# Kernel tuning notes

Hardware: AMD Instinct MI355X
Metric: run time of the kernel (lower is better)

The kernel has to match this reference:

```python
import jax, jax.numpy as jnp
import numpy as np

N = 100000   # n_nodes
E = 1600000  # n_edges (avg degree 16)
IN, HID, OUT = 128, 128, 64


def setup_inputs() -> dict:
    key = jax.random.key(0)
    k0, k1, k2, k3 = jax.random.split(key, 4)
    x = jax.random.normal(k0, (N, IN), dtype=jnp.float32)
    edge_index = jax.random.randint(k1, (2, E), 0, N, dtype=jnp.int32)
    # Glorot-ish init for GCNConv weights, zero bias (PyG default bias=True)
    W1 = jax.random.normal(k2, (IN, HID), dtype=jnp.float32) * (1.0 / np.sqrt(IN))
    b1 = jnp.zeros((HID,), dtype=jnp.float32)
    W2 = jax.random.normal(k3, (HID, OUT), dtype=jnp.float32) * (1.0 / np.sqrt(HID))
    b2 = jnp.zeros((OUT,), dtype=jnp.float32)
    return {"x": x, "W1": W1, "b1": b1, "W2": W2, "b2": b2, "edge_index": edge_index}


def gcn_layer(x, W, b, src, dst):
    """PyG GCNConv: add self-loops, symmetric deg^{-1/2} normalization,
    linear transform, scatter-add aggregation at dst, plus bias."""
    n = x.shape[0]
    h = x @ W                                   # [n, d_out]
    loops = jnp.arange(n, dtype=src.dtype)
    s = jnp.concatenate([src, loops])           # sources incl. self-loops
    d = jnp.concatenate([dst, loops])           # targets incl. self-loops
    deg = jax.ops.segment_sum(jnp.ones_like(d, dtype=h.dtype), d, num_segments=n)
    dinv = jnp.where(deg > 0, jax.lax.rsqrt(deg), 0.0)
    norm = dinv[s] * dinv[d]                    # [E+n]
    msg = h[s] * norm[:, None]                  # gather + scale
    out = jax.ops.segment_sum(msg, d, num_segments=n)  # scatter-add
    return out + b


def reference(x, W1, b1, W2, b2, edge_index):
    src, dst = edge_index[0], edge_index[1]
    h = jax.nn.relu(gcn_layer(x, W1, b1, src, dst))
    return gcn_layer(h, W2, b2, src, dst)
```

## Files before the change

### kernel.cpp

```cpp
#include <hip/hip_runtime.h>

#define NNODES 100000
#define NEDGES 1600000
#define IND 128
#define HIDD 128
#define OUTD 64

#define BSHIFT 8
#define BSIZE  256
#define NBUCK  ((NNODES + BSIZE - 1) / BSIZE)
#define SLACK  4800
#define SEG_CAP 5120
#define BIN_EPB 4096
#define BINB   ((NEDGES + BIN_EPB - 1) / BIN_EPB)
#define WTB    ((IND * HIDD + HIDD * OUTD + 255) / 256)
#define GEMMB  ((NNODES + 127) / 128)

typedef unsigned int  uint32;
typedef __attribute__((ext_vector_type(8))) short short8;
typedef __attribute__((ext_vector_type(4))) float floatx4;
typedef __attribute__((ext_vector_type(4))) unsigned int uivec4;
typedef __attribute__((ext_vector_type(4))) float fvec4;

__device__ __forceinline__ unsigned short f2bf(float f) {
    union { float f; uint32 u; } x; x.f = f;
    uint32 u = x.u;
    return (unsigned short)((u + 0x7fffu + ((u >> 16) & 1u)) >> 16);
}
__device__ __forceinline__ float bflo(uint32 u) {
    union { uint32 i; float f; } x; x.i = u << 16; return x.f;
}
__device__ __forceinline__ float bfhi(uint32 u) {
    union { uint32 i; float f; } x; x.i = u & 0xffff0000u; return x.f;
}

__global__ void k_bin(const int* __restrict__ src, const int* __restrict__ dst,
                      int* __restrict__ bcnt, uint32* __restrict__ staging, int e,
                      const float* __restrict__ W1, const float* __restrict__ W2,
                      unsigned short* __restrict__ wt1, unsigned short* __restrict__ wt2) {
    const int tid = threadIdx.x;
    if (blockIdx.x >= BINB) {
        int idx = (blockIdx.x - BINB) * 256 + tid;
        if (idx < IND * HIDD) {
            int k = idx / HIDD, m = idx - k * HIDD;
            wt1[m * IND + k] = f2bf(W1[idx]);
        } else {
            int j = idx - IND * HIDD;
            if (j < HIDD * OUTD) {
                int k = j / OUTD, m = j - k * OUTD;
                wt2[m * HIDD + k] = f2bf(W2[j]);
            }
        }
        return;
    }

    __shared__ int lh[NBUCK];
    __shared__ int lcur[NBUCK];
    for (int i = tid; i < NBUCK; i += 256) lh[i] = 0;
    __syncthreads();

    const int start = blockIdx.x * BIN_EPB;
    const int4* d4 = (const int4*)dst;
    const int4* s4 = (const int4*)src;

    int4 dv[4], sv[4];
    bool val[4];
#pragma unroll
    for (int k = 0; k < 4; k++) {
        int off = start + 4 * (k * 256 + tid);
        val[k] = off < e;
        if (val[k]) { dv[k] = d4[off >> 2]; sv[k] = s4[off >> 2]; }
    }

#pragma unroll
    for (int k = 0; k < 4; k++) {
        if (val[k]) {
            atomicAdd(&lh[dv[k].x >> BSHIFT], 1);
            atomicAdd(&lh[dv[k].y >> BSHIFT], 1);
            atomicAdd(&lh[dv[k].z >> BSHIFT], 1);
            atomicAdd(&lh[dv[k].w >> BSHIFT], 1);
        }
    }
    __syncthreads();

    for (int i = tid; i < NBUCK; i += 256)
        lcur[i] = lh[i] ? atomicAdd(&bcnt[i], lh[i]) : 0;
    __syncthreads();

#pragma unroll
    for (int k = 0; k < 4; k++) {
        if (val[k]) {
            int d, s, b, pos;
            d = dv[k].x; s = sv[k].x; b = d >> BSHIFT;
            pos = atomicAdd(&lcur[b], 1);
            if (pos < SLACK) staging[b * SLACK + pos] = ((uint32)(d & (BSIZE - 1)) << 17) | (uint32)s;
            d = dv[k].y; s = sv[k].y; b = d >> BSHIFT;
            pos = atomicAdd(&lcur[b], 1);
            if (pos < SLACK) staging[b * SLACK + pos] = ((uint32)(d & (BSIZE - 1)) << 17) | (uint32)s;
            d = dv[k].z; s = sv[k].z; b = d >> BSHIFT;
            pos = atomicAdd(&lcur[b], 1);
            if (pos < SLACK) staging[b * SLACK + pos] = ((uint32)(d & (BSIZE - 1)) << 17) | (uint32)s;
            d = dv[k].w; s = sv[k].w; b = d >> BSHIFT;
            pos = atomicAdd(&lcur[b], 1);
            if (pos < SLACK) staging[b * SLACK + pos] = ((uint32)(d & (BSIZE - 1)) << 17) | (uint32)s;
        }
    }
}

__global__ __launch_bounds__(256)
void k_fill3(const uint32* __restrict__ staging, const int* __restrict__ bcnt,
             int* __restrict__ row_ptr, int* __restrict__ csr_src,
             float* __restrict__ dinv, int n) {
    __shared__ int nc[BSIZE];
    __shared__ int lcur[BSIZE];
    __shared__ int red[256];
    __shared__ int wsum[4];
    __shared__ int seg[SEG_CAP];
    const int b = blockIdx.x;
    const int base = b << BSHIFT;
    const int tid = threadIdx.x;

    nc[tid] = 0;

    int t0 = (tid < b) ? bcnt[tid] : 0;
    int t1 = (tid + 256 < b) ? bcnt[tid + 256] : 0;
    red[tid] = t0 + t1;
    __syncthreads();
    for (int off = 128; off > 0; off >>= 1) {
        if (tid < off) red[tid] += red[tid + off];
        __syncthreads();
    }
    const int r0 = red[0];

    const uint32* st = staging + (size_t)b * SLACK;
    const int cnt = bcnt[b];
    for (int i = tid; i < cnt; i += 256)
        atomicAdd(&nc[st[i] >> 17], 1);
    __syncthreads();

    const int lane = tid & 63;
    const int w = tid >> 6;
    int dg = nc[tid];
    int v = dg;
#pragma unroll
    for (int off = 1; off < 64; off <<= 1) {
        int t = __shfl_up(v, off);
        if (lane >= off) v += t;
    }
    if (lane == 63) wsum[w] = v;
    __syncthreads();
    if (tid == 0) {
        int a = 0;
#pragma unroll
        for (int i = 0; i < 4; i++) { int t = wsum[i]; wsum[i] = a; a += t; }
    }
    __syncthreads();
    const int inc = v + wsum[w];
    const int ex = inc - dg;
    const int vnode = base + tid;
    if (vnode < n) {
        row_ptr[vnode] = r0 + ex;
        dinv[vnode] = rsqrtf((float)(dg + 1));
    }
    lcur[tid] = ex;
    if (b == NBUCK - 1 && tid == 255) row_ptr[n] = r0 + inc;
    __syncthreads();

    for (int i = tid; i < cnt; i += 256) {
        uint32 p = st[i];
        int dl = (int)(p >> 17);
        int s  = (int)(p & 0x1FFFFu);
        int pos = atomicAdd(&lcur[dl], 1);
        if (pos < SEG_CAP) seg[pos] = s;
        else               csr_src[r0 + pos] = s;
    }
    __syncthreads();
    int lim = min(cnt, SEG_CAP);
    for (int i = tid; i < lim; i += 256) csr_src[r0 + i] = seg[i];
}

template<int K, int M, bool ABF16>
__launch_bounds__(512)
__global__ void gemm_mfma(const void* __restrict__ Ap, const unsigned short* __restrict__ WT,
                          const float* __restrict__ dinv, unsigned short* __restrict__ C, int n) {
    constexpr int KP = K + 8;
    constexpr int NT = M / 16;
    __shared__ unsigned short Asl[128 * KP];
    __shared__ unsigned short Wsl[M * KP];

    const int tid = threadIdx.x;
    const int row0 = blockIdx.x * 128;

    {
        constexpr int SEG = (K * 2) / 16;
        const uint4* srcp = (const uint4*)WT;
        for (int idx = tid; idx < M * SEG; idx += 512) {
            int r = idx / SEG, s = idx - r * SEG;
            *(uint4*)(Wsl + r * KP + s * 8) = srcp[idx];
        }
    }
    if constexpr (ABF16) {
        constexpr int U4R = K / 8;
        const unsigned short* Ab = (const unsigned short*)Ap;
        for (int idx = tid; idx < 128 * U4R; idx += 512) {
            int r = idx / U4R, s = idx - r * U4R;
            int grow = row0 + r; if (grow >= n) grow = n - 1;
            *(uint4*)(Asl + r * KP + s * 8) = *(const uint4*)(Ab + (size_t)grow * K + s * 8);
        }
    } else {
        constexpr int F4R = K / 4;
        const float* Af = (const float*)Ap;
        for (int idx = tid; idx < 128 * F4R; idx += 512) {
            int r = idx / F4R, s = idx - r * F4R;
            int grow = row0 + r; if (grow >= n) grow = n - 1;
            float4 v = *(const float4*)(Af + (size_t)grow * K + s * 4);
            uint32 p0 = (uint32)f2bf(v.x) | ((uint32)f2bf(v.y) << 16);
            uint32 p1 = (uint32)f2bf(v.z) | ((uint32)f2bf(v.w) << 16);
            *(uint2*)(Asl + r * KP + s * 4) = make_uint2(p0, p1);
        }
    }
    __syncthreads();

    const int lane = tid & 63;
    const int wave = tid >> 6;
    const int mm = lane & 15;
    const int qq = lane >> 4;

    floatx4 acc[NT];
#pragma unroll
    for (int t = 0; t < NT; t++) acc[t] = (floatx4){0.f, 0.f, 0.f, 0.f};

#pragma unroll
    for (int kc = 0; kc < K / 32; kc++) {
        short8 a = *(const short8*)(Asl + (wave * 16 + mm) * KP + kc * 32 + qq * 8);
#pragma unroll
        for (int t = 0; t < NT; t++) {
            short8 b = *(const short8*)(Wsl + (t * 16 + mm) * KP + kc * 32 + qq * 8);
            acc[t] = __builtin_amdgcn_mfma_f32_16x16x32_bf16(a, b, acc[t], 0, 0, 0);
        }
    }

#pragma unroll
    for (int r = 0; r < 4; r++) {
        int grow = row0 + wave * 16 + qq * 4 + r;
        if (grow < n) {
            float dv = dinv[grow];
#pragma unroll
            for (int t = 0; t < NT; t++)
                C[(size_t)grow * M + t * 16 + mm] = f2bf(acc[t][r] * dv);
        }
    }
}

__launch_bounds__(256)
__global__ void gather_gemm(const unsigned short* __restrict__ h,
                            const int* __restrict__ row_ptr,
                            const int* __restrict__ csr_src,
                            const float* __restrict__ dinv,
                            const float* __restrict__ bias1,
                            const unsigned short* __restrict__ WT2,
                            unsigned short* __restrict__ C2, int n) {
    constexpr int K  = HIDD;
    constexpr int KP = K + 8;
    constexpr int M2 = OUTD;
    __shared__ unsigned short Atl[16 * KP];
    __shared__ unsigned short Wsl[M2 * KP];

    const int tid = threadIdx.x;

    {
        constexpr int SEG = (K * 2) / 16;
        const uint4* srcp = (const uint4*)WT2;
        for (int idx = tid; idx < M2 * SEG; idx += 256) {
            int r = idx / SEG, s = idx - r * SEG;
            *(uint4*)(Wsl + r * KP + s * 8) = srcp[idx];
        }
    }

    const int g = tid >> 4;
    const int l = tid & 15;
    const int v0 = blockIdx.x * 16;
    const int v = v0 + g;

    uint4 pk = make_uint4(0u, 0u, 0u, 0u);
    if (v < n) {
        const float dv = dinv[v];
        float acc[8];
        {
            uint4 u = *(const uint4*)(h + (size_t)v * K + l * 8);
            acc[0] = bflo(u.x); acc[1] = bfhi(u.x);
            acc[2] = bflo(u.y); acc[3] = bfhi(u.y);
            acc[4] = bflo(u.z); acc[5] = bfhi(u.z);
            acc[6] = bflo(u.w); acc[7] = bfhi(u.w);
        }

        int j   = row_ptr[v];
        int end = row_ptr[v + 1];
        for (; j + 3 < end; j += 4) {
            int s0 = csr_src[j];
            int s1 = csr_src[j + 1];
            int s2 = csr_src[j + 2];
            int s3 = csr_src[j + 3];
            uint4 u0 = *(const uint4*)(h + (size_t)s0 * K + l * 8);
            uint4 u1 = *(const uint4*)(h + (size_t)s1 * K + l * 8);
            uint4 u2 = *(const uint4*)(h + (size_t)s2 * K + l * 8);
            uint4 u3 = *(const uint4*)(h + (size_t)s3 * K + l * 8);
            acc[0] += (bflo(u0.x) + bflo(u1.x)) + (bflo(u2.x) + bflo(u3.x));
            acc[1] += (bfhi(u0.x) + bfhi(u1.x)) + (bfhi(u2.x) + bfhi(u3.x));
            acc[2] += (bflo(u0.y) + bflo(u1.y)) + (bflo(u2.y) + bflo(u3.y));
            acc[3] += (bfhi(u0.y) + bfhi(u1.y)) + (bfhi(u2.y) + bfhi(u3.y));
            acc[4] += (bflo(u0.z) + bflo(u1.z)) + (bflo(u2.z) + bflo(u3.z));
            acc[5] += (bfhi(u0.z) + bfhi(u1.z)) + (bfhi(u2.z) + bfhi(u3.z));
            acc[6] += (bflo(u0.w) + bflo(u1.w)) + (bflo(u2.w) + bflo(u3.w));
            acc[7] += (bfhi(u0.w) + bfhi(u1.w)) + (bfhi(u2.w) + bfhi(u3.w));
        }
        for (; j < end; j++) {
            int s0 = csr_src[j];
            uint4 u0 = *(const uint4*)(h + (size_t)s0 * K + l * 8);
            acc[0] += bflo(u0.x); acc[1] += bfhi(u0.x);
            acc[2] += bflo(u0.y); acc[3] += bfhi(u0.y);
            acc[4] += bflo(u0.z); acc[5] += bfhi(u0.z);
            acc[6] += bflo(u0.w); acc[7] += bfhi(u0.w);
        }

#pragma unroll
        for (int i = 0; i < 8; i++) {
            acc[i] = fmaxf(acc[i] * dv + bias1[l * 8 + i], 0.0f);
        }
        pk.x = (uint32)f2bf(acc[0]) | ((uint32)f2bf(acc[1]) << 16);
        pk.y = (uint32)f2bf(acc[2]) | ((uint32)f2bf(acc[3]) << 16);
        pk.z = (uint32)f2bf(acc[4]) | ((uint32)f2bf(acc[5]) << 16);
        pk.w = (uint32)f2bf(acc[6]) | ((uint32)f2bf(acc[7]) << 16);
    }
    *(uint4*)(Atl + g * KP + l * 8) = pk;
    __syncthreads();

    const int lane = tid & 63;
    const int wv = tid >> 6;
    const int mm = lane & 15;
    const int qq = lane >> 4;

    floatx4 o = (floatx4){0.f, 0.f, 0.f, 0.f};
#pragma unroll
    for (int kc = 0; kc < K / 32; kc++) {
        short8 a = *(const short8*)(Atl + mm * KP + kc * 32 + qq * 8);
        short8 b = *(const short8*)(Wsl + (wv * 16 + mm) * KP + kc * 32 + qq * 8);
        o = __builtin_amdgcn_mfma_f32_16x16x32_bf16(a, b, o, 0, 0, 0);
    }

#pragma unroll
    for (int r = 0; r < 4; r++) {
        int grow = v0 + qq * 4 + r;
        if (grow < n) {
            float dv2 = dinv[grow];
            C2[(size_t)grow * M2 + wv * 16 + mm] = f2bf(o[r] * dv2);
        }
    }
}

template<int M, bool RELU, bool OBF16>
__launch_bounds__(256)
__global__ void gather_k(const unsigned short* __restrict__ h,
                         const int* __restrict__ row_ptr,
                         const int* __restrict__ csr_src,
                         const float* __restrict__ dinv,
                         const float* __restrict__ bias,
                         void* __restrict__ outp, int n) {
    constexpr int LPG = M / 8;
    constexpr int GPB = 256 / LPG;
    const int g = threadIdx.x / LPG;
    const int l = threadIdx.x % LPG;
    const int v = blockIdx.x * GPB + g;
    if (v >= n) return;

    const float dv = dinv[v];
    float acc[8];
    {
        uint4 u = *(const uint4*)(h + (size_t)v * M + l * 8);
        acc[0] = bflo(u.x); acc[1] = bfhi(u.x);
        acc[2] = bflo(u.y); acc[3] = bfhi(u.y);
        acc[4] = bflo(u.z); acc[5] = bfhi(u.z);
        acc[6] = bflo(u.w); acc[7] = bfhi(u.w);
    }

    int j   = row_ptr[v];
    int end = row_ptr[v + 1];
    for (; j + 3 < end; j += 4) {
        int s0 = csr_src[j];
        int s1 = csr_src[j + 1];
        int s2 = csr_src[j + 2];
        int s3 = csr_src[j + 3];
        uint4 u0 = *(const uint4*)(h + (size_t)s0 * M + l * 8);
        uint4 u1 = *(const uint4*)(h + (size_t)s1 * M + l * 8);
        uint4 u2 = *(const uint4*)(h + (size_t)s2 * M + l * 8);
        uint4 u3 = *(const uint4*)(h + (size_t)s3 * M + l * 8);
        acc[0] += (bflo(u0.x) + bflo(u1.x)) + (bflo(u2.x) + bflo(u3.x));
        acc[1] += (bfhi(u0.x) + bfhi(u1.x)) + (bfhi(u2.x) + bfhi(u3.x));
        acc[2] += (bflo(u0.y) + bflo(u1.y)) + (bflo(u2.y) + bflo(u3.y));
        acc[3] += (bfhi(u0.y) + bfhi(u1.y)) + (bfhi(u2.y) + bfhi(u3.y));
        acc[4] += (bflo(u0.z) + bflo(u1.z)) + (bflo(u2.z) + bflo(u3.z));
        acc[5] += (bfhi(u0.z) + bfhi(u1.z)) + (bfhi(u2.z) + bfhi(u3.z));
        acc[6] += (bflo(u0.w) + bflo(u1.w)) + (bflo(u2.w) + bflo(u3.w));
        acc[7] += (bfhi(u0.w) + bfhi(u1.w)) + (bfhi(u2.w) + bfhi(u3.w));
    }
    for (; j < end; j++) {
        int s0 = csr_src[j];
        uint4 u0 = *(const uint4*)(h + (size_t)s0 * M + l * 8);
        acc[0] += bflo(u0.x); acc[1] += bfhi(u0.x);
        acc[2] += bflo(u0.y); acc[3] += bfhi(u0.y);
        acc[4] += bflo(u0.z); acc[5] += bfhi(u0.z);
        acc[6] += bflo(u0.w); acc[7] += bfhi(u0.w);
    }

#pragma unroll
    for (int i = 0; i < 8; i++) {
        acc[i] = acc[i] * dv + bias[l * 8 + i];
        if (RELU) acc[i] = fmaxf(acc[i], 0.0f);
    }

    if constexpr (OBF16) {
        uivec4 p;
#pragma unroll
        for (int c = 0; c < 4; c++)
            p[c] = (uint32)f2bf(acc[2 * c]) | ((uint32)f2bf(acc[2 * c + 1]) << 16);
        __builtin_nontemporal_store(p,
            (uivec4*)((unsigned short*)outp + (size_t)v * M + l * 8));
    } else {
        float* op = (float*)outp + (size_t)v * M + l * 8;
        fvec4 a0 = {acc[0], acc[1], acc[2], acc[3]};
        fvec4 a1 = {acc[4], acc[5], acc[6], acc[7]};
        __builtin_nontemporal_store(a0, (fvec4*)op);
        __builtin_nontemporal_store(a1, (fvec4*)(op + 4));
    }
}

extern "C" void kernel_launch(void* const* d_in, const int* in_sizes, int n_in,
                              void* d_out, int out_size, void* d_ws, size_t ws_size,
                              hipStream_t stream) {
    const float* x  = (const float*)d_in[0];
    const float* W1 = (const float*)d_in[1];
    const float* b1 = (const float*)d_in[2];
    const float* W2 = (const float*)d_in[3];
    const float* b2 = (const float*)d_in[4];
    const int*   ei = (const int*)d_in[5];
    const int* src = ei;
    const int* dst = ei + NEDGES;
    float* out = (float*)d_out;

    char* ws = (char*)d_ws;
    float*  dinv    = (float*)ws;   ws += (size_t)NNODES * 4;
    int*    row_ptr = (int*)ws;     ws += (size_t)(NNODES + 4) * 4;
    int*    bcnt    = (int*)ws;     ws += 512 * 4;
    unsigned short* wt1 = (unsigned short*)ws;  ws += (size_t)IND * HIDD * 2;
    unsigned short* wt2 = (unsigned short*)ws;  ws += (size_t)HIDD * OUTD * 2;
    int*    csr_src = (int*)ws;     ws += (size_t)NEDGES * 4;
    uint32* staging = (uint32*)ws;  ws += (size_t)NBUCK * SLACK * 4;
    unsigned short* hbf1 = (unsigned short*)ws; ws += (size_t)NNODES * HIDD * 2;
    unsigned short* hbf2 = (unsigned short*)ws;

    hipMemsetAsync(bcnt, 0, 512 * 4, stream);
    k_bin<<<BINB + WTB, 256, 0, stream>>>(src, dst, bcnt, staging, NEDGES, W1, W2, wt1, wt2);
    k_fill3<<<NBUCK, 256, 0, stream>>>(staging, bcnt, row_ptr, csr_src, dinv, NNODES);

    gemm_mfma<IND, HIDD, false><<<GEMMB, 512, 0, stream>>>(
        x, wt1, dinv, hbf1, NNODES);

    gather_gemm<<<(NNODES + 15) / 16, 256, 0, stream>>>(
        hbf1, row_ptr, csr_src, dinv, b1, wt2, hbf2, NNODES);

    gather_k<OUTD, false, false><<<(NNODES * (OUTD / 8) + 255) / 256, 256, 0, stream>>>(
        hbf2, row_ptr, csr_src, dinv, b2, out, NNODES);
}
```

Baseline: 289.3 us.

## Partition edge binning by bucket group to cut global atomics and scatter

The edge-binning kernel now splits buckets into 8 groups. Each block reads a 16K-edge chunk and keeps only the edges whose bucket falls in its group, staging them in shared memory before reserving global slots and writing to staging. The aim is fewer scattered global writes per block, more contiguous runs per bucket, and smaller shared histograms. The cost is that every edge is read 8 times, and edges past KEEP_CAP (3072 per block) are silently dropped. With uniform random input about 2048 edges land per block, so the cap holds here but is fragile.

```diff
diff --git a/kernel.cpp b/kernel.cpp
--- a/kernel.cpp
+++ b/kernel.cpp
@@ -11,8 +11,12 @@
 #define NBUCK  ((NNODES + BSIZE - 1) / BSIZE)
 #define SLACK  4800
 #define SEG_CAP 5120
-#define BIN_EPB 4096
-#define BINB   ((NEDGES + BIN_EPB - 1) / BIN_EPB)
+#define GRPS   8
+#define NBG    49
+#define EPJ    16384
+#define JB     ((NEDGES + EPJ - 1) / EPJ)
+#define BIN2B  (JB * GRPS)
+#define KEEP_CAP 3072
 #define WTB    ((IND * HIDD + HIDD * OUTD + 255) / 256)
 #define GEMMB  ((NNODES + 127) / 128)
 
@@ -39,8 +43,8 @@
                       const float* __restrict__ W1, const float* __restrict__ W2,
                       unsigned short* __restrict__ wt1, unsigned short* __restrict__ wt2) {
     const int tid = threadIdx.x;
-    if (blockIdx.x >= BINB) {
-        int idx = (blockIdx.x - BINB) * 256 + tid;
+    if (blockIdx.x >= BIN2B) {
+        int idx = (blockIdx.x - BIN2B) * 256 + tid;
         if (idx < IND * HIDD) {
             int k = idx / HIDD, m = idx - k * HIDD;
             wt1[m * IND + k] = f2bf(W1[idx]);
@@ -54,56 +58,60 @@
         return;
     }
 
-    __shared__ int lh[NBUCK];
-    __shared__ int lcur[NBUCK];
-    for (int i = tid; i < NBUCK; i += 256) lh[i] = 0;
-    __syncthreads();
-
-    const int start = blockIdx.x * BIN_EPB;
+    __shared__ int lh[NBG];
+    __shared__ int lcur[NBG];
+    __shared__ int nk;
+    __shared__ uint32 keep[KEEP_CAP];
+
+    const int g = blockIdx.x & 7;
+    const int j = blockIdx.x >> 3;
+
+    for (int i = tid; i < NBG; i += 256) lh[i] = 0;
+    if (tid == 0) nk = 0;
+    __syncthreads();
+
+    const int start = j * EPJ;
+    const int end = min(start + EPJ, e);
     const int4* d4 = (const int4*)dst;
     const int4* s4 = (const int4*)src;
 
-    int4 dv[4], sv[4];
-    bool val[4];
-#pragma unroll
-    for (int k = 0; k < 4; k++) {
-        int off = start + 4 * (k * 256 + tid);
-        val[k] = off < e;
-        if (val[k]) { dv[k] = d4[off >> 2]; sv[k] = s4[off >> 2]; }
-    }
-
-#pragma unroll
-    for (int k = 0; k < 4; k++) {
-        if (val[k]) {
-            atomicAdd(&lh[dv[k].x >> BSHIFT], 1);
-            atomicAdd(&lh[dv[k].y >> BSHIFT], 1);
-            atomicAdd(&lh[dv[k].z >> BSHIFT], 1);
-            atomicAdd(&lh[dv[k].w >> BSHIFT], 1);
-        }
-    }
-    __syncthreads();
-
-    for (int i = tid; i < NBUCK; i += 256)
-        lcur[i] = lh[i] ? atomicAdd(&bcnt[i], lh[i]) : 0;
-    __syncthreads();
-
-#pragma unroll
-    for (int k = 0; k < 4; k++) {
-        if (val[k]) {
-            int d, s, b, pos;
-            d = dv[k].x; s = sv[k].x; b = d >> BSHIFT;
-            pos = atomicAdd(&lcur[b], 1);
-            if (pos < SLACK) staging[b * SLACK + pos] = ((uint32)(d & (BSIZE - 1)) << 17) | (uint32)s;
-            d = dv[k].y; s = sv[k].y; b = d >> BSHIFT;
-            pos = atomicAdd(&lcur[b], 1);
-            if (pos < SLACK) staging[b * SLACK + pos] = ((uint32)(d & (BSIZE - 1)) << 17) | (uint32)s;
-            d = dv[k].z; s = sv[k].z; b = d >> BSHIFT;
-            pos = atomicAdd(&lcur[b], 1);
-            if (pos < SLACK) staging[b * SLACK + pos] = ((uint32)(d & (BSIZE - 1)) << 17) | (uint32)s;
-            d = dv[k].w; s = sv[k].w; b = d >> BSHIFT;
-            pos = atomicAdd(&lcur[b], 1);
-            if (pos < SLACK) staging[b * SLACK + pos] = ((uint32)(d & (BSIZE - 1)) << 17) | (uint32)s;
-        }
+    for (int off = start + 4 * tid; off < end; off += 1024) {
+        int4 dv = d4[off >> 2];
+        int4 sv = s4[off >> 2];
+#define PROC(DD, SS)                                                          \
+        {                                                                     \
+            int d = (DD), s = (SS);                                           \
+            int b = d >> BSHIFT;                                              \
+            if ((b & 7) == g) {                                               \
+                int k = atomicAdd(&nk, 1);                                    \
+                if (k < KEEP_CAP) {                                           \
+                    atomicAdd(&lh[b >> 3], 1);                                \
+                    keep[k] = ((uint32)(b >> 3) << 25) |                      \
+                              ((uint32)(d & (BSIZE - 1)) << 17) | (uint32)s;  \
+                }                                                             \
+            }                                                                 \
+        }
+        PROC(dv.x, sv.x)
+        PROC(dv.y, sv.y)
+        PROC(dv.z, sv.z)
+        PROC(dv.w, sv.w)
+#undef PROC
+    }
+    __syncthreads();
+
+    for (int i = tid; i < NBG; i += 256) {
+        int b = (i << 3) | g;
+        lcur[i] = (b < NBUCK && lh[i]) ? atomicAdd(&bcnt[b], lh[i]) : 0;
+    }
+    __syncthreads();
+
+    const int kn = min(nk, KEEP_CAP);
+    for (int k = tid; k < kn; k += 256) {
+        uint32 e2 = keep[k];
+        int i = (int)(e2 >> 25);
+        int pos = atomicAdd(&lcur[i], 1);
+        if (pos < SLACK)
+            staging[(size_t)((i << 3) | g) * SLACK + pos] = e2 & 0x1FFFFFFu;
     }
 }
 
@@ -459,7 +467,7 @@
     unsigned short* hbf2 = (unsigned short*)ws;
 
     hipMemsetAsync(bcnt, 0, 512 * 4, stream);
-    k_bin<<<BINB + WTB, 256, 0, stream>>>(src, dst, bcnt, staging, NEDGES, W1, W2, wt1, wt2);
+    k_bin<<<BIN2B + WTB, 256, 0, stream>>>(src, dst, bcnt, staging, NEDGES, W1, W2, wt1, wt2);
     k_fill3<<<NBUCK, 256, 0, stream>>>(staging, bcnt, row_ptr, csr_src, dinv, NNODES);
 
     gemm_mfma<IND, HIDD, false><<<GEMMB, 512, 0, stream>>>(
```

Result: slower. 302.1 us (+4.4%).

## Fuse first-layer GEMM into binning kernel and move source dinv scaling into gather

Applied to the files above, without the earlier changes.

The first-layer x@W1 GEMM now runs as extra blocks of the edge-binning kernel, so it no longer waits for the CSR build and dinv. Because dinv is not yet available there, the source-side normalization moves into the layer-1 gather, which loads dinv[src] per edge and multiplies. Each GEMM block also converts and transposes W1 into shared memory itself, replacing the separate wt1 pass. The trade-off is an extra scattered dinv load and multiply per edge in the gather, plus redundant W1 conversion in every GEMM block.

```diff
diff --git a/kernel.cpp b/kernel.cpp
--- a/kernel.cpp
+++ b/kernel.cpp
@@ -13,8 +13,8 @@
 #define SEG_CAP 5120
 #define BIN_EPB 4096
 #define BINB   ((NEDGES + BIN_EPB - 1) / BIN_EPB)
-#define WTB    ((IND * HIDD + HIDD * OUTD + 255) / 256)
 #define GEMMB  ((NNODES + 127) / 128)
+#define WT2B   ((HIDD * OUTD + 511) / 512)
 
 typedef unsigned int  uint32;
 typedef __attribute__((ext_vector_type(8))) short short8;
@@ -34,75 +34,133 @@
     union { uint32 i; float f; } x; x.i = u & 0xffff0000u; return x.f;
 }
 
-__global__ void k_bin(const int* __restrict__ src, const int* __restrict__ dst,
-                      int* __restrict__ bcnt, uint32* __restrict__ staging, int e,
-                      const float* __restrict__ W1, const float* __restrict__ W2,
-                      unsigned short* __restrict__ wt1, unsigned short* __restrict__ wt2) {
+__launch_bounds__(512)
+__global__ void k_bin_gemm(const int* __restrict__ src, const int* __restrict__ dst,
+                           int* __restrict__ bcnt, uint32* __restrict__ staging, int e,
+                           const float* __restrict__ x, const float* __restrict__ W1,
+                           const float* __restrict__ W2, unsigned short* __restrict__ wt2,
+                           unsigned short* __restrict__ C, int n) {
+    constexpr int K = IND;
+    constexpr int KP = K + 8;
+    constexpr int M = HIDD;
+    constexpr int NT = M / 16;
+    __shared__ __align__(16) char smem[2 * 128 * KP * 2];
+
     const int tid = threadIdx.x;
-    if (blockIdx.x >= BINB) {
-        int idx = (blockIdx.x - BINB) * 256 + tid;
-        if (idx < IND * HIDD) {
-            int k = idx / HIDD, m = idx - k * HIDD;
-            wt1[m * IND + k] = f2bf(W1[idx]);
-        } else {
-            int j = idx - IND * HIDD;
-            if (j < HIDD * OUTD) {
-                int k = j / OUTD, m = j - k * OUTD;
-                wt2[m * HIDD + k] = f2bf(W2[j]);
+    const int bid = blockIdx.x;
+
+    if (bid < BINB) {
+        int* lh   = (int*)smem;
+        int* lcur = lh + NBUCK;
+        for (int i = tid; i < NBUCK; i += 512) lh[i] = 0;
+        __syncthreads();
+
+        const int start = bid * BIN_EPB;
+        const int4* d4 = (const int4*)dst;
+        const int4* s4 = (const int4*)src;
+
+        int4 dv[2], sv[2];
+        bool val[2];
+#pragma unroll
+        for (int k = 0; k < 2; k++) {
+            int off = start + 4 * (k * 512 + tid);
+            val[k] = off < e;
+            if (val[k]) { dv[k] = d4[off >> 2]; sv[k] = s4[off >> 2]; }
+        }
+
+#pragma unroll
+        for (int k = 0; k < 2; k++) {
+            if (val[k]) {
+                atomicAdd(&lh[dv[k].x >> BSHIFT], 1);
+                atomicAdd(&lh[dv[k].y >> BSHIFT], 1);
+                atomicAdd(&lh[dv[k].z >> BSHIFT], 1);
+                atomicAdd(&lh[dv[k].w >> BSHIFT], 1);
             }
         }
+        __syncthreads();
+
+        for (int i = tid; i < NBUCK; i += 512)
+            lcur[i] = lh[i] ? atomicAdd(&bcnt[i], lh[i]) : 0;
+        __syncthreads();
+
+#pragma unroll
+        for (int k = 0; k < 2; k++) {
+            if (val[k]) {
+                int d, s, b, pos;
+                d = dv[k].x; s = sv[k].x; b = d >> BSHIFT;
+                pos = atomicAdd(&lcur[b], 1);
+                if (pos < SLACK) staging[(size_t)b * SLACK + pos] = ((uint32)(d & (BSIZE - 1)) << 17) | (uint32)s;
+                d = dv[k].y; s = sv[k].y; b = d >> BSHIFT;
+                pos = atomicAdd(&lcur[b], 1);
+                if (pos < SLACK) staging[(size_t)b * SLACK + pos] = ((uint32)(d & (BSIZE - 1)) << 17) | (uint32)s;
+                d = dv[k].z; s = sv[k].z; b = d >> BSHIFT;
+                pos = atomicAdd(&lcur[b], 1);
+                if (pos < SLACK) staging[(size_t)b * SLACK + pos] = ((uint32)(d & (BSIZE - 1)) << 17) | (uint32)s;
+                d = dv[k].w; s = sv[k].w; b = d >> BSHIFT;
+                pos = atomicAdd(&lcur[b], 1);
+                if (pos < SLACK) staging[(size_t)b * SLACK + pos] = ((uint32)(d & (BSIZE - 1)) << 17) | (uint32)s;
+            }
+        }
         return;
     }
 
-    __shared__ int lh[NBUCK];
-    __shared__ int lcur[NBUCK];
-    for (int i = tid; i < NBUCK; i += 256) lh[i] = 0;
-    __syncthreads();
-
-    const int start = blockIdx.x * BIN_EPB;
-    const int4* d4 = (const int4*)dst;
-    const int4* s4 = (const int4*)src;
-
-    int4 dv[4], sv[4];
-    bool val[4];
-#pragma unroll
-    for (int k = 0; k < 4; k++) {
-        int off = start + 4 * (k * 256 + tid);
-        val[k] = off < e;
-        if (val[k]) { dv[k] = d4[off >> 2]; sv[k] = s4[off >> 2]; }
-    }
-
-#pragma unroll
-    for (int k = 0; k < 4; k++) {
-        if (val[k]) {
-            atomicAdd(&lh[dv[k].x >> BSHIFT], 1);
-            atomicAdd(&lh[dv[k].y >> BSHIFT], 1);
-            atomicAdd(&lh[dv[k].z >> BSHIFT], 1);
-            atomicAdd(&lh[dv[k].w >> BSHIFT], 1);
-        }
-    }
-    __syncthreads();
-
-    for (int i = tid; i < NBUCK; i += 256)
-        lcur[i] = lh[i] ? atomicAdd(&bcnt[i], lh[i]) : 0;
-    __syncthreads();
-
-#pragma unroll
-    for (int k = 0; k < 4; k++) {
-        if (val[k]) {
-            int d, s, b, pos;
-            d = dv[k].x; s = sv[k].x; b = d >> BSHIFT;
-            pos = atomicAdd(&lcur[b], 1);
-            if (pos < SLACK) staging[b * SLACK + pos] = ((uint32)(d & (BSIZE - 1)) << 17) | (uint32)s;
-            d = dv[k].y; s = sv[k].y; b = d >> BSHIFT;
-            pos = atomicAdd(&lcur[b], 1);
-            if (pos < SLACK) staging[b * SLACK + pos] = ((uint32)(d & (BSIZE - 1)) << 17) | (uint32)s;
-            d = dv[k].z; s = sv[k].z; b = d >> BSHIFT;
-            pos = atomicAdd(&lcur[b], 1);
-            if (pos < SLACK) staging[b * SLACK + pos] = ((uint32)(d & (BSIZE - 1)) << 17) | (uint32)s;
-            d = dv[k].w; s = sv[k].w; b = d >> BSHIFT;
-            pos = atomicAdd(&lcur[b], 1);
-            if (pos < SLACK) staging[b * SLACK + pos] = ((uint32)(d & (BSIZE - 1)) << 17) | (uint32)s;
+    if (bid >= BINB + GEMMB) {
+        int idx = (bid - BINB - GEMMB) * 512 + tid;
+        if (idx < HIDD * OUTD) {
+            int k = idx / OUTD, m = idx - k * OUTD;
+            wt2[m * HIDD + k] = f2bf(W2[idx]);
+        }
+        return;
+    }
+
+    unsigned short* Asl = (unsigned short*)smem;
+    unsigned short* Wsl = Asl + 128 * KP;
+
+    const int row0 = (bid - BINB) * 128;
+
+    for (int idx = tid; idx < 128 * 128; idx += 512) {
+        int k = idx >> 7, m = idx & 127;
+        Wsl[m * KP + k] = f2bf(W1[idx]);
+    }
+    {
+        constexpr int F4R = K / 4;
+        for (int idx = tid; idx < 128 * F4R; idx += 512) {
+            int r = idx / F4R, s = idx - r * F4R;
+            int grow = row0 + r; if (grow >= n) grow = n - 1;
+            float4 v = *(const float4*)(x + (size_t)grow * K + s * 4);
+            uint32 p0 = (uint32)f2bf(v.x) | ((uint32)f2bf(v.y) << 16);
+            uint32 p1 = (uint32)f2bf(v.z) | ((uint32)f2bf(v.w) << 16);
+            *(uint2*)(Asl + r * KP + s * 4) = make_uint2(p0, p1);
+        }
+    }
+    __syncthreads();
+
+    const int lane = tid & 63;
+    const int wave = tid >> 6;
+    const int mm = lane & 15;
+    const int qq = lane >> 4;
+
+    floatx4 acc[NT];
+#pragma unroll
+    for (int t = 0; t < NT; t++) acc[t] = (floatx4){0.f, 0.f, 0.f, 0.f};
+
+#pragma unroll
+    for (int kc = 0; kc < K / 32; kc++) {
+        short8 a = *(const short8*)(Asl + (wave * 16 + mm) * KP + kc * 32 + qq * 8);
+#pragma unroll
+        for (int t = 0; t < NT; t++) {
+            short8 b = *(const short8*)(Wsl + (t * 16 + mm) * KP + kc * 32 + qq * 8);
+            acc[t] = __builtin_amdgcn_mfma_f32_16x16x32_bf16(a, b, acc[t], 0, 0, 0);
+        }
+    }
+
+#pragma unroll
+    for (int r = 0; r < 4; r++) {
+        int grow = row0 + wave * 16 + qq * 4 + r;
+        if (grow < n) {
+#pragma unroll
+            for (int t = 0; t < NT; t++)
+                C[(size_t)grow * M + t * 16 + mm] = f2bf(acc[t][r]);
         }
     }
 }
@@ -177,79 +235,6 @@
     __syncthreads();
     int lim = min(cnt, SEG_CAP);
     for (int i = tid; i < lim; i += 256) csr_src[r0 + i] = seg[i];
-}
-
-template<int K, int M, bool ABF16>
-__launch_bounds__(512)
-__global__ void gemm_mfma(const void* __restrict__ Ap, const unsigned short* __restrict__ WT,
-                          const float* __restrict__ dinv, unsigned short* __restrict__ C, int n) {
-    constexpr int KP = K + 8;
-    constexpr int NT = M / 16;
-    __shared__ unsigned short Asl[128 * KP];
-    __shared__ unsigned short Wsl[M * KP];
-
-    const int tid = threadIdx.x;
-    const int row0 = blockIdx.x * 128;
-
-    {
-        constexpr int SEG = (K * 2) / 16;
-        const uint4* srcp = (const uint4*)WT;
-        for (int idx = tid; idx < M * SEG; idx += 512) {
-            int r = idx / SEG, s = idx - r * SEG;
-            *(uint4*)(Wsl + r * KP + s * 8) = srcp[idx];
-        }
-    }
-    if constexpr (ABF16) {
-        constexpr int U4R = K / 8;
-        const unsigned short* Ab = (const unsigned short*)Ap;
-        for (int idx = tid; idx < 128 * U4R; idx += 512) {
-            int r = idx / U4R, s = idx - r * U4R;
-            int grow = row0 + r; if (grow >= n) grow = n - 1;
-            *(uint4*)(Asl + r * KP + s * 8) = *(const uint4*)(Ab + (size_t)grow * K + s * 8);
-        }
-    } else {
-        constexpr int F4R = K / 4;
-        const float* Af = (const float*)Ap;
-        for (int idx = tid; idx < 128 * F4R; idx += 512) {
-            int r = idx / F4R, s = idx - r * F4R;
-            int grow = row0 + r; if (grow >= n) grow = n - 1;
-            float4 v = *(const float4*)(Af + (size_t)grow * K + s * 4);
-            uint32 p0 = (uint32)f2bf(v.x) | ((uint32)f2bf(v.y) << 16);
-            uint32 p1 = (uint32)f2bf(v.z) | ((uint32)f2bf(v.w) << 16);
-            *(uint2*)(Asl + r * KP + s * 4) = make_uint2(p0, p1);
-        }
-    }
-    __syncthreads();
-
-    const int lane = tid & 63;
-    const int wave = tid >> 6;
-    const int mm = lane & 15;
-    const int qq = lane >> 4;
-
-    floatx4 acc[NT];
-#pragma unroll
-    for (int t = 0; t < NT; t++) acc[t] = (floatx4){0.f, 0.f, 0.f, 0.f};
-
-#pragma unroll
-    for (int kc = 0; kc < K / 32; kc++) {
-        short8 a = *(const short8*)(Asl + (wave * 16 + mm) * KP + kc * 32 + qq * 8);
-#pragma unroll
-        for (int t = 0; t < NT; t++) {
-            short8 b = *(const short8*)(Wsl + (t * 16 + mm) * KP + kc * 32 + qq * 8);
-            acc[t] = __builtin_amdgcn_mfma_f32_16x16x32_bf16(a, b, acc[t], 0, 0, 0);
-        }
-    }
-
-#pragma unroll
-    for (int r = 0; r < 4; r++) {
-        int grow = row0 + wave * 16 + qq * 4 + r;
-        if (grow < n) {
-            float dv = dinv[grow];
-#pragma unroll
-            for (int t = 0; t < NT; t++)
-                C[(size_t)grow * M + t * 16 + mm] = f2bf(acc[t][r] * dv);
-        }
-    }
 }
 
 __launch_bounds__(256)
@@ -288,10 +273,10 @@
         float acc[8];
         {
             uint4 u = *(const uint4*)(h + (size_t)v * K + l * 8);
-            acc[0] = bflo(u.x); acc[1] = bfhi(u.x);
-            acc[2] = bflo(u.y); acc[3] = bfhi(u.y);
-            acc[4] = bflo(u.z); acc[5] = bfhi(u.z);
-            acc[6] = bflo(u.w); acc[7] = bfhi(u.w);
+            acc[0] = dv * bflo(u.x); acc[1] = dv * bfhi(u.x);
+            acc[2] = dv * bflo(u.y); acc[3] = dv * bfhi(u.y);
+            acc[4] = dv * bflo(u.z); acc[5] = dv * bfhi(u.z);
+            acc[6] = dv * bflo(u.w); acc[7] = dv * bfhi(u.w);
         }
 
         int j   = row_ptr[v];
@@ -301,26 +286,28 @@
             int s1 = csr_src[j + 1];
             int s2 = csr_src[j + 2];
             int s3 = csr_src[j + 3];
+            float q0 = dinv[s0], q1 = dinv[s1], q2 = dinv[s2], q3 = dinv[s3];
             uint4 u0 = *(const uint4*)(h + (size_t)s0 * K + l * 8);
             uint4 u1 = *(const uint4*)(h + (size_t)s1 * K + l * 8);
             uint4 u2 = *(const uint4*)(h + (size_t)s2 * K + l * 8);
             uint4 u3 = *(const uint4*)(h + (size_t)s3 * K + l * 8);
-            acc[0] += (bflo(u0.x) + bflo(u1.x)) + (bflo(u2.x) + bflo(u3.x));
-            acc[1] += (bfhi(u0.x) + bfhi(u1.x)) + (bfhi(u2.x) + bfhi(u3.x));
-            acc[2] += (bflo(u0.y) + bflo(u1.y)) + (bflo(u2.y) + bflo(u3.y));
-            acc[3] += (bfhi(u0.y) + bfhi(u1.y)) + (bfhi(u2.y) + bfhi(u3.y));
-            acc[4] += (bflo(u0.z) + bflo(u1.z)) + (bflo(u2.z) + bflo(u3.z));
-            acc[5] += (bfhi(u0.z) + bfhi(u1.z)) + (bfhi(u2.z) + bfhi(u3.z));
-            acc[6] += (bflo(u0.w) + bflo(u1.w)) + (bflo(u2.w) + bflo(u3.w));
-            acc[7] += (bfhi(u0.w) + bfhi(u1.w)) + (bfhi(u2.w) + bfhi(u3.w));
+            acc[0] += (q0 * bflo(u0.x) + q1 * bflo(u1.x)) + (q2 * bflo(u2.x) + q3 * bflo(u3.x));
+            acc[1] += (q0 * bfhi(u0.x) + q1 * bfhi(u1.x)) + (q2 * bfhi(u2.x) + q3 * bfhi(u3.x));
+            acc[2] += (q0 * bflo(u0.y) + q1 * bflo(u1.y)) + (q2 * bflo(u2.y) + q3 * bflo(u3.y));
+            acc[3] += (q0 * bfhi(u0.y) + q1 * bfhi(u1.y)) + (q2 * bfhi(u2.y) + q3 * bfhi(u3.y));
+            acc[4] += (q0 * bflo(u0.z) + q1 * bflo(u1.z)) + (q2 * bflo(u2.z) + q3 * bflo(u3.z));
+            acc[5] += (q0 * bfhi(u0.z) + q1 * bfhi(u1.z)) + (q2 * bfhi(u2.z) + q3 * bfhi(u3.z));
+            acc[6] += (q0 * bflo(u0.w) + q1 * bflo(u1.w)) + (q2 * bflo(u2.w) + q3 * bflo(u3.w));
+            acc[7] += (q0 * bfhi(u0.w) + q1 * bfhi(u1.w)) + (q2 * bfhi(u2.w) + q3 * bfhi(u3.w));
         }
         for (; j < end; j++) {
             int s0 = csr_src[j];
+            float q0 = dinv[s0];
             uint4 u0 = *(const uint4*)(h + (size_t)s0 * K + l * 8);
-            acc[0] += bflo(u0.x); acc[1] += bfhi(u0.x);
-            acc[2] += bflo(u0.y); acc[3] += bfhi(u0.y);
-            acc[4] += bflo(u0.z); acc[5] += bfhi(u0.z);
-            acc[6] += bflo(u0.w); acc[7] += bfhi(u0.w);
+            acc[0] += q0 * bflo(u0.x); acc[1] += q0 * bfhi(u0.x);
+            acc[2] += q0 * bflo(u0.y); acc[3] += q0 * bfhi(u0.y);
+            acc[4] += q0 * bflo(u0.z); acc[5] += q0 * bfhi(u0.z);
+            acc[6] += q0 * bflo(u0.w); acc[7] += q0 * bfhi(u0.w);
         }
 
 #pragma unroll
@@ -451,7 +438,6 @@
     float*  dinv    = (float*)ws;   ws += (size_t)NNODES * 4;
     int*    row_ptr = (int*)ws;     ws += (size_t)(NNODES + 4) * 4;
     int*    bcnt    = (int*)ws;     ws += 512 * 4;
-    unsigned short* wt1 = (unsigned short*)ws;  ws += (size_t)IND * HIDD * 2;
     unsigned short* wt2 = (unsigned short*)ws;  ws += (size_t)HIDD * OUTD * 2;
     int*    csr_src = (int*)ws;     ws += (size_t)NEDGES * 4;
     uint32* staging = (uint32*)ws;  ws += (size_t)NBUCK * SLACK * 4;
@@ -459,11 +445,10 @@
     unsigned short* hbf2 = (unsigned short*)ws;
 
     hipMemsetAsync(bcnt, 0, 512 * 4, stream);
-    k_bin<<<BINB + WTB, 256, 0, stream>>>(src, dst, bcnt, staging, NEDGES, W1, W2, wt1, wt2);
+    k_bin_gemm<<<BINB + GEMMB + WT2B, 512, 0, stream>>>(
+        src, dst, bcnt, staging, NEDGES, x, W1, W2, wt2, hbf1, NNODES);
+
     k_fill3<<<NBUCK, 256, 0, stream>>>(staging, bcnt, row_ptr, csr_src, dinv, NNODES);
-
-    gemm_mfma<IND, HIDD, false><<<GEMMB, 512, 0, stream>>>(
-        x, wt1, dinv, hbf1, NNODES);
 
     gather_gemm<<<(NNODES + 15) / 16, 256, 0, stream>>>(
         hbf1, row_ptr, csr_src, dinv, b1, wt2, hbf2, NNODES);
```

Result: no change. 286.6 us (-0.9%).
